# Kernel optimization log

Hardware: AMD Instinct MI355X
Metric: run time of the kernel (lower is better)

The kernel has to match this reference:

```python
import jax, jax.numpy as jnp
import numpy as np

NODE_NUM = 6
C_IN = 1024
B = 16384
N_OPS = 9
TAU = 10.0
EPS = 1e-5
ACTS = (jax.nn.relu, jax.nn.sigmoid, jnp.tanh)


def setup_inputs() -> dict:
    key = jax.random.key(0)
    k = jax.random.split(key, 12)
    n_edges = NODE_NUM * (NODE_NUM + 1) // 2  # 21
    nB = n_edges - NODE_NUM  # 15 edges with cin=cout=C_IN//2

    def w(kk, shape, fan_in):
        return jax.random.normal(kk, shape, jnp.float32) / np.float32(np.sqrt(fan_in))

    return {
        "x": jax.random.normal(k[0], (B, C_IN), jnp.float32),
        "arch_params": 0.001 * jax.random.normal(k[1], (n_edges, N_OPS), jnp.float32),
        "gumbel": jax.random.gumbel(k[2], (n_edges, N_OPS), jnp.float32),
        "dense_w_A": w(k[3], (NODE_NUM, 3, C_IN // 2, C_IN), C_IN),
        "dense_b_A": 0.01 * jax.random.normal(k[4], (NODE_NUM, 3, C_IN // 2), jnp.float32),
        "group_w_A": w(k[5], (NODE_NUM, 3, 4, C_IN // 8, C_IN // 4), C_IN // 4),
        "group_b_A": 0.01 * jax.random.normal(k[6], (NODE_NUM, 3, C_IN // 2), jnp.float32),
        "pool_w_A": w(k[7], (NODE_NUM, 2, C_IN // 2, C_IN), C_IN),
        "dense_w_B": w(k[8], (nB, 3, C_IN // 2, C_IN // 2), C_IN // 2),
        "dense_b_B": 0.01 * jax.random.normal(k[9], (nB, 3, C_IN // 2), jnp.float32),
        "group_w_B": w(k[10], (nB, 3, 4, C_IN // 8, C_IN // 8), C_IN // 8),
        "group_b_B": 0.01 * jax.random.normal(k[11], (nB, 3, C_IN // 2), jnp.float32),
    }


def _batchnorm(h):
    # training-mode BatchNorm2d on [B, C, 1, 1] == normalize over batch, affine-free
    m = jnp.mean(h, axis=0, keepdims=True)
    v = jnp.var(h, axis=0, keepdims=True)
    return (h - m) * jax.lax.rsqrt(v + EPS)


def _apply_edge(h, op_idx, wscale, dw, db, gw, gb, pw):
    # h: [B, cin]; dw: [3, cout, cin]; gw: [3, 4, cout//4, cin//4]; pw: [2, cout, cin] or None
    cout = dw.shape[1]

    def pool(p):
        def f(hh):
            # ReLU-Conv1x1-BN preprocess when cin != cout, else identity
            y = _batchnorm(jax.nn.relu(hh) @ pw[p].T) if pw is not None else hh
            if p == 0:  # avg_pool_3x3 on 1x1 spatial, pad=1, count_include_pad
                y = y / 9.0
            # p == 1: max_pool_3x3 on 1x1 spatial is identity
            return _batchnorm(y)  # MixedOp-appended BatchNorm2d(affine=False)
        return f

    def dense(a):
        return lambda hh: ACTS[a](hh @ dw[a].T + db[a])

    def gdense(a):
        def f(hh):
            hg = hh.reshape(hh.shape[0], 4, -1)  # [B, 4, cin//4]
            y = jnp.einsum('bgi,goi->bgo', hg, gw[a]).reshape(hh.shape[0], -1) + gb[a]
            return ACTS[a](y)
        return f

    zero = lambda hh: jnp.zeros((hh.shape[0], cout), hh.dtype)
    branches = [pool(0), pool(1), dense(0), dense(1), dense(2),
                gdense(0), gdense(1), gdense(2), zero]
    return jax.lax.switch(op_idx, branches, h) * wscale


def reference(x, arch_params, gumbel, dense_w_A, dense_b_A, group_w_A, group_b_A,
              pool_w_A, dense_w_B, dense_b_B, group_w_B, group_b_B):
    # GDAS gumbel-softmax hard routing (straight-through)
    logits = (jax.nn.log_softmax(arch_params, axis=1) + gumbel) / TAU
    prob = jax.nn.softmax(logits, axis=1)
    index = jnp.argmax(prob, axis=1)                      # [n_edges]
    one_h = jax.nn.one_hot(index, N_OPS, dtype=prob.dtype)
    hardwts = one_h - jax.lax.stop_gradient(prob) + prob  # [n_edges, N_OPS]

    # arch rows are indexed by sorted edge-key order, matching torch edge2index
    keys = sorted('{}->{}'.format(j, i + 1) for i in range(NODE_NUM) for j in range(i + 1))
    e2i = {kk: n for n, kk in enumerate(keys)}

    states = [x]
    a_ct = 0
    b_ct = 0
    for i in range(1, NODE_NUM + 1):
        acc = None
        for j in range(i):
            e = e2i['{}->{}'.format(j, i)]
            w_e = hardwts[e, index[e]]
            if j == 0:
                out = _apply_edge(states[0], index[e], w_e, dense_w_A[a_ct], dense_b_A[a_ct],
                                  group_w_A[a_ct], group_b_A[a_ct], pool_w_A[a_ct])
                a_ct += 1
            else:
                out = _apply_edge(states[j], index[e], w_e, dense_w_B[b_ct], dense_b_B[b_ct],
                                  group_w_B[b_ct], group_b_B[b_ct], None)
                b_ct += 1
            acc = out if acc is None else acc + out
        states.append(acc)
    return states[-1]  # [B, C_IN//2]; final_linear is never applied in forward()
```

## Files before the change

kernel.cpp:

```cpp
#include <hip/hip_runtime.h>

#define BATCH 16384
#define CH 512
#define EPSBN 1e-5f

typedef __attribute__((ext_vector_type(8))) short short8;
typedef __attribute__((ext_vector_type(4))) float f32x4;
typedef __attribute__((ext_vector_type(4))) unsigned short ushort4v;

#define GLOAD16(gp, lp) __builtin_amdgcn_global_load_lds( \
    (const __attribute__((address_space(1))) void*)(gp),  \
    (__attribute__((address_space(3))) void*)(lp), 16, 0, 0)

__constant__ int d_etab[6][6] = {
  {0,0,0,0,0,0},
  {1,6,0,0,0,0},
  {2,7,11,0,0,0},
  {3,8,12,15,0,0},
  {4,9,13,16,18,0},
  {5,10,14,17,19,20}};
__constant__ int d_bct[21] = {0,0,0,0,0,0, 0,1,3,6,10, 2,4,7,11, 5,8,12, 9,13, 14};

static __device__ __forceinline__ long woff(int e){
  return (e < 6) ? (long)e*524288 : 3145728L + (long)d_bct[e]*262144;
}

static __device__ __forceinline__ unsigned short f2b(float f){
  union { float f; unsigned u; } v; v.f = f;
  unsigned r = v.u + 0x7fffu + ((v.u >> 16) & 1u);
  return (unsigned short)(r >> 16);
}
static __device__ __forceinline__ float b2f(unsigned short u){
  union { unsigned u; float f; } v; v.u = ((unsigned)u) << 16; return v.f;
}
static __device__ __forceinline__ float actf(int act, float v){
  if (act == 0) return fmaxf(v, 0.f);
  if (act == 1) return 1.f/(1.f + __expf(-v));
  float e = __expf(2.f*v);
  return 1.f - 2.f/(e + 1.f);
}

static __device__ __forceinline__ void col_stats_atomic(
    float vs, float vq, int cn, int slot, float* partw){
  vs += __shfl_xor(vs, 16); vs += __shfl_xor(vs, 32);
  vq += __shfl_xor(vq, 16); vq += __shfl_xor(vq, 32);
  if (((threadIdx.x) & 63) < 16){
    atomicAdd(&partw[((long)slot*CH + cn)*2    ], vs);
    atomicAdd(&partw[((long)slot*CH + cn)*2 + 1], vq);
  }
}

static __device__ __forceinline__ void ms_from(const float* part, int slot, int cn,
                                               float& mu, float& var){
  long sl = ((long)slot*CH + cn)*2;
  float s = part[sl], q = part[sl+1];
  mu = s * (1.f/16384.f);
  var = fmaxf(q * (1.f/16384.f) - mu*mu, 0.f);
}
static __device__ __forceinline__ float alphaA(int id, float v){
  float s1r = rsqrtf(v + EPSBN);
  float vz = v / (v + EPSBN);
  return (id==0) ? (s1r * (1.f/9.f) * rsqrtf(vz*(1.f/81.f) + EPSBN))
                 : (s1r * rsqrtf(vz + EPSBN));
}
static __device__ __forceinline__ float alphaB(int id, float v){
  return (id==0) ? ((1.f/9.f) * rsqrtf(v*(1.f/81.f) + EPSBN))
                 : rsqrtf(v + EPSBN);
}

__global__ void k_sentinel(float* out){ out[0] = 1.0e6f; }

__global__ void k_index(const float* __restrict__ ap, const float* __restrict__ gum,
                        int* __restrict__ idx, float* __restrict__ wsc){
  int e = threadIdx.x;
  if (e >= 21) return;
  const float* a = ap + e*9;
  const float* g = gum + e*9;
  float m = a[0];
  for (int o=1;o<9;o++) m = fmaxf(m, a[o]);
  float s = 0.f;
  for (int o=0;o<9;o++) s += expf(a[o]-m);
  float lse = m + logf(s);
  float lg[9]; float lm = -1e30f;
  for (int o=0;o<9;o++){ lg[o] = (a[o]-lse+g[o]) / 10.0f; lm = fmaxf(lm, lg[o]); }
  float ss = 0.f;
  for (int o=0;o<9;o++) ss += expf(lg[o]-lm);
  int bi = 0; float bp = -1.f;
  for (int o=0;o<9;o++){
    float p = expf(lg[o]-lm)/ss;
    if (p > bp){ bp = p; bi = o; }
  }
  idx[e] = bi;
  wsc[e] = (1.0f - bp) + bp;
}

__global__ void k_f2b4(const float* __restrict__ in, unsigned short* __restrict__ outp, long n4){
  long stride = (long)gridDim.x*blockDim.x;
  for (long i = (long)blockIdx.x*blockDim.x + threadIdx.x; i < n4; i += stride){
    const float4 v = ((const float4*)in)[i];
    ushort4v o;
    o[0] = f2b(v.x); o[1] = f2b(v.y); o[2] = f2b(v.z); o[3] = f2b(v.w);
    ((ushort4v*)outp)[i] = o;
  }
}

__global__ void k_wconv_all(const int* __restrict__ idxp,
                            const float* __restrict__ dwA, const float* __restrict__ pwA,
                            const float* __restrict__ gwA, const float* __restrict__ dwB,
                            const float* __restrict__ gwB,
                            unsigned short* __restrict__ Wball){
  int e = blockIdx.x >> 7;
  int blk = blockIdx.x & 127;
  int id = idxp[e];
  const float* src; long n;
  if (e < 6){
    int a = e;
    if (id >= 2 && id <= 4){ n = 524288; src = dwA + ((long)a*3 + (id-2))*n; }
    else if (id < 2)       { n = 524288; src = pwA + ((long)a*2 + id)*n; }
    else if (id <= 7)      { n = 131072; src = gwA + ((long)a*3 + (id-5))*131072; }
    else return;
  } else {
    int b = d_bct[e];
    if (id >= 2 && id <= 4)     { n = 262144; src = dwB + ((long)b*3 + (id-2))*n; }
    else if (id >= 5 && id <= 7){ n = 65536;  src = gwB + ((long)b*3 + (id-5))*65536; }
    else return;
  }
  unsigned short* dst = Wball + woff(e);
  long n4 = n >> 2;
  long stride = 128*256;
  for (long i = (long)blk*256 + threadIdx.x; i < n4; i += stride){
    const float4 v = ((const float4*)src)[i];
    ushort4v o;
    o[0] = f2b(v.x); o[1] = f2b(v.y); o[2] = f2b(v.z); o[3] = f2b(v.w);
    ((ushort4v*)dst)[i] = o;
  }
}

__global__ __launch_bounds__(512, 4) void k_gemmA_all(
    const unsigned short* __restrict__ xb, const unsigned short* __restrict__ Wball,
    unsigned short* __restrict__ s0, unsigned short* __restrict__ s1,
    unsigned short* __restrict__ s2, unsigned short* __restrict__ s3,
    unsigned short* __restrict__ s4, unsigned short* __restrict__ pre6,
    const float* __restrict__ dbA, const float* __restrict__ gbA,
    const int* __restrict__ idxp, const float* __restrict__ wscp,
    float* __restrict__ partw)
{
  int e = blockIdx.x >> 9;
  int id = idxp[e];
  if (id == 8) return;
  unsigned short* target;
  switch(e){ case 0: target=s0; break; case 1: target=s1; break; case 2: target=s2; break;
             case 3: target=s3; break; case 4: target=s4; break; default: target=pre6; }
  bool pool = (id < 2);
  bool grp = (id >= 5);
  int K = grp ? 256 : 1024;
  int act = pool ? 0 : (grp ? id-5 : id-2);
  float we = wscp[e];

  int inner = blockIdx.x & 511;
  int lg = (inner & 7) * 64 + (inner >> 3);
  int rowTile = lg >> 2, colTile = lg & 3;
  int row0 = rowTile * 128, col0 = colTile * 128;

  int t = threadIdx.x;
  int lane = t & 63, wave = t >> 6;
  int wm = wave >> 2, wn = wave & 3;
  int l16 = lane & 15, lq = lane >> 4;

  __shared__ unsigned short LDS[24576];

  int ra = t >> 2;
  int ca = (((t & 3) ^ ((ra >> 1) & 3)) << 3);
  int aoff[4], boff[2];
  #pragma unroll
  for (int m=0;m<4;m++){ int R = wm*64 + m*16 + l16; aoff[m] = R*32 + ((lq ^ ((R>>1)&3))<<3); }
  #pragma unroll
  for (int n=0;n<2;n++){ int C = wn*32 + n*16 + l16; boff[n] = C*32 + ((lq ^ ((C>>1)&3))<<3); }

  const unsigned short* Abase = xb + (grp ? (long)colTile*K : 0);
  const unsigned short* Wbase = Wball + (long)e*524288 + (long)col0*K;
  const unsigned short* gA = Abase + (long)(row0 + ra)*1024 + ca;
  const unsigned short* gB = Wbase + (long)ra*K + ca;
  const float* bias = (grp ? gbA : dbA) + ((long)e*3 + act)*CH;

  f32x4 acc[4][2];
  #pragma unroll
  for (int m=0;m<4;m++){ acc[m][0]=(f32x4){0,0,0,0}; acc[m][1]=(f32x4){0,0,0,0}; }

  auto STAGE = [&](int tile, int bsel){
    long kk = (long)tile*32;
    GLOAD16(gA + kk, &LDS[bsel*4096 + t*8]);
    GLOAD16(gB + kk, &LDS[12288 + bsel*4096 + t*8]);
  };

  int nk = K >> 5;
  STAGE(0, 0);
  STAGE(1, 1);
  int cb = 0;
  for (int kt = 0; kt < nk; ++kt){
    if (kt+1 < nk) { asm volatile("s_waitcnt vmcnt(2)" ::: "memory"); }
    else           { asm volatile("s_waitcnt vmcnt(0)" ::: "memory"); }
    __builtin_amdgcn_s_barrier();
    if (kt+2 < nk) STAGE(kt+2, (cb >= 1) ? cb-1 : cb+2);
    const unsigned short* pA = &LDS[cb*4096];
    const unsigned short* pB = &LDS[12288 + cb*4096];
    short8 a[4], b[2];
    #pragma unroll
    for (int m=0;m<4;m++){
      a[m] = *(const short8*)(pA + aoff[m]);
      if (pool){
        #pragma unroll
        for (int q=0;q<8;q++) a[m][q] = (a[m][q] < (short)0) ? (short)0 : a[m][q];
      }
    }
    #pragma unroll
    for (int n=0;n<2;n++) b[n] = *(const short8*)(pB + boff[n]);
    #pragma unroll
    for (int m=0;m<4;m++)
      #pragma unroll
      for (int n=0;n<2;n++)
        acc[m][n] = __builtin_amdgcn_mfma_f32_16x16x32_bf16(a[m], b[n], acc[m][n], 0,0,0);
    cb = (cb+1 == 3) ? 0 : cb+1;
  }

  #pragma unroll
  for (int n=0;n<2;n++){
    int cn = col0 + wn*32 + n*16 + l16;
    float bv = pool ? 0.f : bias[cn];
    float cs = 0.f, cq = 0.f;
    #pragma unroll
    for (int m=0;m<4;m++)
      #pragma unroll
      for (int r=0;r<4;r++){
        int row = row0 + wm*64 + m*16 + lq*4 + r;
        long off = (long)row*CH + cn;
        float v = pool ? acc[m][n][r] : (we * actf(act, acc[m][n][r] + bv));
        target[off] = f2b(v);
        cs += v; cq += v*v;
      }
    col_stats_atomic(cs, cq, cn, e, partw);
  }
}

__global__ __launch_bounds__(512, 4) void k_fix1(
    unsigned short* __restrict__ s1, const float* __restrict__ part,
    float* __restrict__ partw, const int* __restrict__ idxp,
    const float* __restrict__ wscp)
{
  int id = idxp[0];
  float we = wscp[0];

  int bid = blockIdx.x;
  int lg = (bid & 7) * 64 + (bid >> 3);
  int rowTile = lg >> 2, colTile = lg & 3;
  int row0 = rowTile * 128, col0 = colTile * 128;

  int t = threadIdx.x;
  int lane = t & 63, wave = t >> 6;
  int wm = wave >> 2, wn = wave & 3;
  int l16 = lane & 15, lq = lane >> 4;

  #pragma unroll
  for (int n=0;n<2;n++){
    int cn = col0 + wn*32 + n*16 + l16;
    float cs = 0.f, cq = 0.f;
    float mu = 0.f, al = 0.f;
    if (id < 2){
      float var; ms_from(part, 0, cn, mu, var);
      al = alphaA(id, var);
    }
    #pragma unroll
    for (int m=0;m<4;m++)
      #pragma unroll
      for (int r=0;r<4;r++){
        int row = row0 + wm*64 + m*16 + lq*4 + r;
        long off = (long)row*CH + cn;
        float v;
        if (id == 8){ v = 0.f; s1[off] = 0; }
        else if (id < 2){ v = we * (b2f(s1[off]) - mu) * al; s1[off] = f2b(v); }
        else { v = b2f(s1[off]); }
        cs += v; cq += v*v;
      }
    col_stats_atomic(cs, cq, cn, 6+1, partw);
  }
}

__global__ __launch_bounds__(512, 4) void k_fused(
    int node,
    const unsigned short* __restrict__ pre,
    const unsigned short* __restrict__ sb0, const unsigned short* __restrict__ sb1,
    const unsigned short* __restrict__ sb2, const unsigned short* __restrict__ sb3,
    const unsigned short* __restrict__ sb4,
    unsigned short* __restrict__ sbout, float* __restrict__ outf,
    const unsigned short* __restrict__ Wball,
    const float* __restrict__ dbB, const float* __restrict__ gbB,
    const float* __restrict__ part, float* __restrict__ partw,
    const int* __restrict__ idxp, const float* __restrict__ wscp)
{
  int bid = blockIdx.x;
  int lg = (bid & 7) * 64 + (bid >> 3);
  int rowTile = lg >> 2, colTile = lg & 3;
  int row0 = rowTile * 128, col0 = colTile * 128;

  int t = threadIdx.x;
  int lane = t & 63, wave = t >> 6;
  int wm = wave >> 2, wn = wave & 3;
  int l16 = lane & 15, lq = lane >> 4;

  __shared__ unsigned short LDS[24576];

  int ra = t >> 2;
  int ca = (((t & 3) ^ ((ra >> 1) & 3)) << 3);
  int aoff[4], boff[2];
  #pragma unroll
  for (int m=0;m<4;m++){ int R = wm*64 + m*16 + l16; aoff[m] = R*32 + ((lq ^ ((R>>1)&3))<<3); }
  #pragma unroll
  for (int n=0;n<2;n++){ int C = wn*32 + n*16 + l16; boff[n] = C*32 + ((lq ^ ((C>>1)&3))<<3); }

  f32x4 facc[4][2];
  #pragma unroll
  for (int m=0;m<4;m++){ facc[m][0]=(f32x4){0,0,0,0}; facc[m][1]=(f32x4){0,0,0,0}; }

  for (int jj = 0; jj < node; ++jj){
    int e = d_etab[node-1][jj];
    int id = idxp[e];
    if (id == 8) continue;
    float we = wscp[e];

    if (jj == 0){
      if (id < 2){
        #pragma unroll
        for (int n=0;n<2;n++){
          int cn = col0 + wn*32 + n*16 + l16;
          float mu, var; ms_from(part, e, cn, mu, var);
          float al = alphaA(id, var);
          #pragma unroll
          for (int m=0;m<4;m++){
            int rowb = row0 + wm*64 + m*16 + lq*4;
            #pragma unroll
            for (int r=0;r<4;r++)
              facc[m][n][r] += we * (b2f(pre[(long)(rowb+r)*CH + cn]) - mu) * al;
          }
        }
      } else {
        #pragma unroll
        for (int n=0;n<2;n++){
          int cn = col0 + wn*32 + n*16 + l16;
          #pragma unroll
          for (int m=0;m<4;m++){
            int rowb = row0 + wm*64 + m*16 + lq*4;
            #pragma unroll
            for (int r=0;r<4;r++)
              facc[m][n][r] += b2f(pre[(long)(rowb+r)*CH + cn]);
          }
        }
      }
      continue;
    }

    const unsigned short* st;
    switch(jj){ case 1: st=sb0; break; case 2: st=sb1; break;
                case 3: st=sb2; break; case 4: st=sb3; break; default: st=sb4; }

    if (id < 2){
      #pragma unroll
      for (int n=0;n<2;n++){
        int cn = col0 + wn*32 + n*16 + l16;
        float mu, var; ms_from(part, 6+jj, cn, mu, var);
        float al = alphaB(id, var);
        #pragma unroll
        for (int m=0;m<4;m++){
          int rowb = row0 + wm*64 + m*16 + lq*4;
          #pragma unroll
          for (int r=0;r<4;r++)
            facc[m][n][r] += we * (b2f(st[(long)(rowb+r)*CH + cn]) - mu) * al;
        }
      }
      continue;
    }

    bool grp = (id >= 5);
    int K = grp ? 128 : 512;
    int act = grp ? id - 5 : id - 2;
    const unsigned short* Abase = st + (grp ? (long)colTile*K : 0);
    const unsigned short* Wbase = Wball + woff(e) + (long)col0*K;
    const float* bias = (grp ? gbB : dbB) + ((long)d_bct[e]*3 + act)*CH;

    const unsigned short* gA = Abase + (long)(row0 + ra)*512 + ca;
    const unsigned short* gB = Wbase + (long)ra*K + ca;

    f32x4 acc[4][2];
    #pragma unroll
    for (int m=0;m<4;m++){ acc[m][0]=(f32x4){0,0,0,0}; acc[m][1]=(f32x4){0,0,0,0}; }

    auto STAGE = [&](int tile, int bsel){
      long kk = (long)tile*32;
      GLOAD16(gA + kk, &LDS[bsel*4096 + t*8]);
      GLOAD16(gB + kk, &LDS[12288 + bsel*4096 + t*8]);
    };

    int nk = K >> 5;
    __builtin_amdgcn_s_barrier();
    STAGE(0, 0);
    STAGE(1, 1);
    int cb = 0;
    for (int kt = 0; kt < nk; ++kt){
      if (kt+1 < nk) { asm volatile("s_waitcnt vmcnt(2)" ::: "memory"); }
      else           { asm volatile("s_waitcnt vmcnt(0)" ::: "memory"); }
      __builtin_amdgcn_s_barrier();
      if (kt+2 < nk) STAGE(kt+2, (cb >= 1) ? cb-1 : cb+2);
      const unsigned short* pA = &LDS[cb*4096];
      const unsigned short* pB = &LDS[12288 + cb*4096];
      short8 a[4], b[2];
      #pragma unroll
      for (int m=0;m<4;m++) a[m] = *(const short8*)(pA + aoff[m]);
      #pragma unroll
      for (int n=0;n<2;n++) b[n] = *(const short8*)(pB + boff[n]);
      #pragma unroll
      for (int m=0;m<4;m++)
        #pragma unroll
        for (int n=0;n<2;n++)
          acc[m][n] = __builtin_amdgcn_mfma_f32_16x16x32_bf16(a[m], b[n], acc[m][n], 0,0,0);
      cb = (cb+1 == 3) ? 0 : cb+1;
    }

    #pragma unroll
    for (int n=0;n<2;n++){
      int cn = col0 + wn*32 + n*16 + l16;
      float bv = bias[cn];
      #pragma unroll
      for (int m=0;m<4;m++)
        #pragma unroll
        for (int r=0;r<4;r++)
          facc[m][n][r] += we * actf(act, acc[m][n][r] + bv);
    }
  }

  #pragma unroll
  for (int n=0;n<2;n++){
    int cn = col0 + wn*32 + n*16 + l16;
    float cs = 0.f, cq = 0.f;
    #pragma unroll
    for (int m=0;m<4;m++){
      int rowb = row0 + wm*64 + m*16 + lq*4;
      #pragma unroll
      for (int r=0;r<4;r++){
        long off = (long)(rowb+r)*CH + cn;
        float v = facc[m][n][r];
        if (node == 6) outf[off] = v;
        else { sbout[off] = f2b(v); cs += v; cq += v*v; }
      }
    }
    if (node < 6) col_stats_atomic(cs, cq, cn, 6+node, partw);
  }
}

extern "C" void kernel_launch(void* const* d_in, const int* in_sizes, int n_in,
                              void* d_out, int out_size, void* d_ws, size_t ws_size,
                              hipStream_t stream)
{
  const float* x   = (const float*)d_in[0];
  const float* ap  = (const float*)d_in[1];
  const float* gum = (const float*)d_in[2];
  const float* dwA = (const float*)d_in[3];
  const float* dbA = (const float*)d_in[4];
  const float* gwA = (const float*)d_in[5];
  const float* gbA = (const float*)d_in[6];
  const float* pwA = (const float*)d_in[7];
  const float* dwB = (const float*)d_in[8];
  const float* dbB = (const float*)d_in[9];
  const float* gwB = (const float*)d_in[10];
  const float* gbB = (const float*)d_in[11];
  float* out = (float*)d_out;

  char* ws = (char*)d_ws;
  size_t cur = 0;
  auto alloc = [&](size_t bytes)->void*{
    size_t o = cur; cur += (bytes + 255) & ~(size_t)255; return (void*)(ws + o);
  };
  int*   idx  = (int*)  alloc(21*sizeof(int));
  float* wsc  = (float*)alloc(21*sizeof(float));
  float* part = (float*)alloc((size_t)12*CH*2*sizeof(float));
  unsigned short* Wball = (unsigned short*)alloc((size_t)7077888*sizeof(unsigned short));
  unsigned short* pre6  = (unsigned short*)alloc((size_t)BATCH*CH*sizeof(unsigned short));
  unsigned short* xb    = (unsigned short*)alloc((size_t)BATCH*1024*sizeof(unsigned short));
  unsigned short* sb[5];
  for (int i=0;i<5;i++)
    sb[i] = (unsigned short*)alloc((size_t)BATCH*CH*sizeof(unsigned short));

  if (cur > ws_size){
    hipLaunchKernelGGL(k_sentinel, dim3(1), dim3(1), 0, stream, out);
    return;
  }

  hipMemsetAsync(part, 0, (size_t)12*CH*2*sizeof(float), stream);
  hipLaunchKernelGGL(k_f2b4, dim3(2048), dim3(256), 0, stream, x, xb, (long)BATCH*1024/4);
  hipLaunchKernelGGL(k_index, dim3(1), dim3(32), 0, stream, ap, gum, idx, wsc);
  hipLaunchKernelGGL(k_wconv_all, dim3(21*128), dim3(256), 0, stream,
                     idx, dwA, pwA, gwA, dwB, gwB, Wball);

  hipLaunchKernelGGL(k_gemmA_all, dim3(6*512), dim3(512), 0, stream,
                     xb, Wball, sb[0], sb[1], sb[2], sb[3], sb[4], pre6,
                     dbA, gbA, idx, wsc, part);
  hipLaunchKernelGGL(k_fix1, dim3(512), dim3(512), 0, stream,
                     sb[0], part, part, idx, wsc);

  for (int node = 2; node <= 6; node++){
    const unsigned short* pre = (node < 6) ? sb[node-1] : pre6;
    unsigned short* sbout = (node < 6) ? sb[node-1] : sb[0] ;
    hipLaunchKernelGGL(k_fused, dim3(512), dim3(512), 0, stream,
                       node, pre, sb[0], sb[1], sb[2], sb[3], sb[4],
                       sbout, out, Wball, dbB, gbB, part, part, idx, wsc);
  }
}
```

Baseline: 426.5 us.

## Enlarge gemmA tile to 256x128 with BK=64 and interleaved staged loads

```diff
diff --git a/kernel.cpp b/kernel.cpp
--- a/kernel.cpp
+++ b/kernel.cpp
@@ -136,7 +136,7 @@
   }
 }
 
-__global__ __launch_bounds__(512, 4) void k_gemmA_all(
+__global__ __launch_bounds__(512, 2) void k_gemmA_all(
     const unsigned short* __restrict__ xb, const unsigned short* __restrict__ Wball,
     unsigned short* __restrict__ s0, unsigned short* __restrict__ s1,
     unsigned short* __restrict__ s2, unsigned short* __restrict__ s3,
@@ -145,7 +145,7 @@
     const int* __restrict__ idxp, const float* __restrict__ wscp,
     float* __restrict__ partw)
 {
-  int e = blockIdx.x >> 9;
+  int e = blockIdx.x >> 8;
   int id = idxp[e];
   if (id == 8) return;
   unsigned short* target;
@@ -157,84 +157,167 @@
   int act = pool ? 0 : (grp ? id-5 : id-2);
   float we = wscp[e];
 
-  int inner = blockIdx.x & 511;
-  int lg = (inner & 7) * 64 + (inner >> 3);
+  int inner = blockIdx.x & 255;
+  int lg = (inner & 7) * 32 + (inner >> 3);
   int rowTile = lg >> 2, colTile = lg & 3;
-  int row0 = rowTile * 128, col0 = colTile * 128;
+  int row0 = rowTile * 256, col0 = colTile * 128;
 
   int t = threadIdx.x;
   int lane = t & 63, wave = t >> 6;
   int wm = wave >> 2, wn = wave & 3;
   int l16 = lane & 15, lq = lane >> 4;
 
-  __shared__ unsigned short LDS[24576];
-
-  int ra = t >> 2;
-  int ca = (((t & 3) ^ ((ra >> 1) & 3)) << 3);
-  int aoff[4], boff[2];
-  #pragma unroll
-  for (int m=0;m<4;m++){ int R = wm*64 + m*16 + l16; aoff[m] = R*32 + ((lq ^ ((R>>1)&3))<<3); }
-  #pragma unroll
-  for (int n=0;n<2;n++){ int C = wn*32 + n*16 + l16; boff[n] = C*32 + ((lq ^ ((C>>1)&3))<<3); }
-
-  const unsigned short* Abase = xb + (grp ? (long)colTile*K : 0);
-  const unsigned short* Wbase = Wball + (long)e*524288 + (long)col0*K;
-  const unsigned short* gA = Abase + (long)(row0 + ra)*1024 + ca;
-  const unsigned short* gB = Wbase + (long)ra*K + ca;
-  const float* bias = (grp ? gbA : dbA) + ((long)e*3 + act)*CH;
-
-  f32x4 acc[4][2];
-  #pragma unroll
-  for (int m=0;m<4;m++){ acc[m][0]=(f32x4){0,0,0,0}; acc[m][1]=(f32x4){0,0,0,0}; }
-
-  auto STAGE = [&](int tile, int bsel){
-    long kk = (long)tile*32;
-    GLOAD16(gA + kk, &LDS[bsel*4096 + t*8]);
-    GLOAD16(gB + kk, &LDS[12288 + bsel*4096 + t*8]);
+  __shared__ unsigned short LDS[73728];
+
+  int srow = t >> 3;
+  int schunk = (t & 7) ^ (srow & 7);
+  const unsigned short* gA = xb + (grp ? (long)colTile*K : 0)
+                              + (long)(row0 + srow)*1024 + schunk*8;
+  const unsigned short* gB = Wball + (long)e*524288 + (long)col0*K
+                              + (long)srow*K + schunk*8;
+
+  int aoff[8][2], boff[2][2];
+  #pragma unroll
+  for (int mf=0; mf<8; mf++){
+    int R = wm*128 + mf*16 + l16;
+    #pragma unroll
+    for (int kh=0; kh<2; kh++)
+      aoff[mf][kh] = R*64 + (((kh<<2)|lq) ^ (R&7))*8;
+  }
+  #pragma unroll
+  for (int nf=0; nf<2; nf++){
+    int C = wn*32 + nf*16 + l16;
+    #pragma unroll
+    for (int kh=0; kh<2; kh++)
+      boff[nf][kh] = 16384 + C*64 + (((kh<<2)|lq) ^ (C&7))*8;
+  }
+
+  f32x4 acc[8][2];
+  #pragma unroll
+  for (int mf=0; mf<8; mf++){ acc[mf][0]=(f32x4){0,0,0,0}; acc[mf][1]=(f32x4){0,0,0,0}; }
+
+  auto STAGE_A = [&](int tt, int tb, int i){
+    GLOAD16(gA + (long)tt*64 + (long)i*65536, &LDS[tb*24576 + i*4096 + t*8]);
   };
-
-  int nk = K >> 5;
-  STAGE(0, 0);
-  STAGE(1, 1);
+  auto STAGE_B = [&](int tt, int tb, int i){
+    GLOAD16(gB + (long)tt*64 + (long)i*64*K, &LDS[tb*24576 + 16384 + i*4096 + t*8]);
+  };
+
+  int nk = K >> 6;
+  #pragma unroll
+  for (int i=0;i<4;i++) STAGE_A(0,0,i);
+  #pragma unroll
+  for (int i=0;i<2;i++) STAGE_B(0,0,i);
+  #pragma unroll
+  for (int i=0;i<4;i++) STAGE_A(1,1,i);
+  #pragma unroll
+  for (int i=0;i<2;i++) STAGE_B(1,1,i);
+
   int cb = 0;
   for (int kt = 0; kt < nk; ++kt){
-    if (kt+1 < nk) { asm volatile("s_waitcnt vmcnt(2)" ::: "memory"); }
+    if (kt+1 < nk) { asm volatile("s_waitcnt vmcnt(6)" ::: "memory"); }
     else           { asm volatile("s_waitcnt vmcnt(0)" ::: "memory"); }
     __builtin_amdgcn_s_barrier();
-    if (kt+2 < nk) STAGE(kt+2, (cb >= 1) ? cb-1 : cb+2);
-    const unsigned short* pA = &LDS[cb*4096];
-    const unsigned short* pB = &LDS[12288 + cb*4096];
+    const unsigned short* buf = &LDS[cb*24576];
+    int tt = kt + 2;
+    int tb = (cb >= 1) ? cb-1 : cb+2;
+    bool st = (tt < nk);
+
     short8 a[4], b[2];
+    b[0] = *(const short8*)(buf + boff[0][0]);
+    b[1] = *(const short8*)(buf + boff[1][0]);
+    a[0] = *(const short8*)(buf + aoff[0][0]);
+    a[1] = *(const short8*)(buf + aoff[1][0]);
+    a[2] = *(const short8*)(buf + aoff[2][0]);
+    a[3] = *(const short8*)(buf + aoff[3][0]);
+    if (pool){
+      #pragma unroll
+      for (int m=0;m<4;m++)
+        #pragma unroll
+        for (int q=0;q<8;q++) a[m][q] = (a[m][q] < (short)0) ? (short)0 : a[m][q];
+    }
+    if (st){ STAGE_A(tt,tb,0); STAGE_A(tt,tb,1); }
+    __builtin_amdgcn_s_setprio(1);
     #pragma unroll
     for (int m=0;m<4;m++){
-      a[m] = *(const short8*)(pA + aoff[m]);
-      if (pool){
+      acc[m][0] = __builtin_amdgcn_mfma_f32_16x16x32_bf16(a[m], b[0], acc[m][0], 0,0,0);
+      acc[m][1] = __builtin_amdgcn_mfma_f32_16x16x32_bf16(a[m], b[1], acc[m][1], 0,0,0);
+    }
+    __builtin_amdgcn_s_setprio(0);
+    __builtin_amdgcn_s_barrier();
+    a[0] = *(const short8*)(buf + aoff[4][0]);
+    a[1] = *(const short8*)(buf + aoff[5][0]);
+    a[2] = *(const short8*)(buf + aoff[6][0]);
+    a[3] = *(const short8*)(buf + aoff[7][0]);
+    if (pool){
+      #pragma unroll
+      for (int m=0;m<4;m++)
         #pragma unroll
         for (int q=0;q<8;q++) a[m][q] = (a[m][q] < (short)0) ? (short)0 : a[m][q];
-      }
-    }
-    #pragma unroll
-    for (int n=0;n<2;n++) b[n] = *(const short8*)(pB + boff[n]);
-    #pragma unroll
-    for (int m=0;m<4;m++)
-      #pragma unroll
-      for (int n=0;n<2;n++)
-        acc[m][n] = __builtin_amdgcn_mfma_f32_16x16x32_bf16(a[m], b[n], acc[m][n], 0,0,0);
+    }
+    if (st){ STAGE_A(tt,tb,2); STAGE_A(tt,tb,3); }
+    __builtin_amdgcn_s_setprio(1);
+    #pragma unroll
+    for (int m=0;m<4;m++){
+      acc[4+m][0] = __builtin_amdgcn_mfma_f32_16x16x32_bf16(a[m], b[0], acc[4+m][0], 0,0,0);
+      acc[4+m][1] = __builtin_amdgcn_mfma_f32_16x16x32_bf16(a[m], b[1], acc[4+m][1], 0,0,0);
+    }
+    __builtin_amdgcn_s_setprio(0);
+    __builtin_amdgcn_s_barrier();
+    b[0] = *(const short8*)(buf + boff[0][1]);
+    b[1] = *(const short8*)(buf + boff[1][1]);
+    a[0] = *(const short8*)(buf + aoff[0][1]);
+    a[1] = *(const short8*)(buf + aoff[1][1]);
+    a[2] = *(const short8*)(buf + aoff[2][1]);
+    a[3] = *(const short8*)(buf + aoff[3][1]);
+    if (pool){
+      #pragma unroll
+      for (int m=0;m<4;m++)
+        #pragma unroll
+        for (int q=0;q<8;q++) a[m][q] = (a[m][q] < (short)0) ? (short)0 : a[m][q];
+    }
+    if (st){ STAGE_B(tt,tb,0); }
+    __builtin_amdgcn_s_setprio(1);
+    #pragma unroll
+    for (int m=0;m<4;m++){
+      acc[m][0] = __builtin_amdgcn_mfma_f32_16x16x32_bf16(a[m], b[0], acc[m][0], 0,0,0);
+      acc[m][1] = __builtin_amdgcn_mfma_f32_16x16x32_bf16(a[m], b[1], acc[m][1], 0,0,0);
+    }
+    __builtin_amdgcn_s_setprio(0);
+    __builtin_amdgcn_s_barrier();
+    a[0] = *(const short8*)(buf + aoff[4][1]);
+    a[1] = *(const short8*)(buf + aoff[5][1]);
+    a[2] = *(const short8*)(buf + aoff[6][1]);
+    a[3] = *(const short8*)(buf + aoff[7][1]);
+    if (pool){
+      #pragma unroll
+      for (int m=0;m<4;m++)
+        #pragma unroll
+        for (int q=0;q<8;q++) a[m][q] = (a[m][q] < (short)0) ? (short)0 : a[m][q];
+    }
+    if (st){ STAGE_B(tt,tb,1); }
+    __builtin_amdgcn_s_setprio(1);
+    #pragma unroll
+    for (int m=0;m<4;m++){
+      acc[4+m][0] = __builtin_amdgcn_mfma_f32_16x16x32_bf16(a[m], b[0], acc[4+m][0], 0,0,0);
+      acc[4+m][1] = __builtin_amdgcn_mfma_f32_16x16x32_bf16(a[m], b[1], acc[4+m][1], 0,0,0);
+    }
+    __builtin_amdgcn_s_setprio(0);
     cb = (cb+1 == 3) ? 0 : cb+1;
   }
 
   #pragma unroll
-  for (int n=0;n<2;n++){
-    int cn = col0 + wn*32 + n*16 + l16;
-    float bv = pool ? 0.f : bias[cn];
+  for (int nf=0; nf<2; nf++){
+    int cn = col0 + wn*32 + nf*16 + l16;
+    float bv = pool ? 0.f : ((grp ? gbA : dbA) + ((long)e*3 + act)*CH)[cn];
     float cs = 0.f, cq = 0.f;
     #pragma unroll
-    for (int m=0;m<4;m++)
+    for (int mf=0; mf<8; mf++)
       #pragma unroll
       for (int r=0;r<4;r++){
-        int row = row0 + wm*64 + m*16 + lq*4 + r;
+        int row = row0 + wm*128 + mf*16 + lq*4 + r;
         long off = (long)row*CH + cn;
-        float v = pool ? acc[m][n][r] : (we * actf(act, acc[m][n][r] + bv));
+        float v = pool ? acc[mf][nf][r] : (we * actf(act, acc[mf][nf][r] + bv));
         target[off] = f2b(v);
         cs += v; cq += v*v;
       }
@@ -499,7 +582,7 @@
   hipLaunchKernelGGL(k_wconv_all, dim3(21*128), dim3(256), 0, stream,
                      idx, dwA, pwA, gwA, dwB, gwB, Wball);
 
-  hipLaunchKernelGGL(k_gemmA_all, dim3(6*512), dim3(512), 0, stream,
+  hipLaunchKernelGGL(k_gemmA_all, dim3(6*256), dim3(512), 0, stream,
                      xb, Wball, sb[0], sb[1], sb[2], sb[3], sb[4], pre6,
                      dbA, gbA, idx, wsc, part);
   hipLaunchKernelGGL(k_fix1, dim3(512), dim3(512), 0, stream,
```

Result: slower. 447.2 us (+4.9%).
